# Performance work log

Measured on AMD Instinct MI355X. Metric: run time of the kernel, lower is better.

The kernel has to match this reference:

```python
import jax, jax.numpy as jnp
import numpy as np

N_NODES = 50000
N_EDGES = 400000
LATENT = 128
HIDDEN = 512
N_HEADS = 2          # latent // 64, NodeAttn default num_heads
HEAD_DIM = LATENT // N_HEADS
N_GRAPHS = 500
LN_EPS = 1e-5


def setup_inputs() -> dict:
    key = jax.random.key(0)
    ks = jax.random.split(key, 24)
    s = 0.02
    inp = {
        "edges": jax.random.randint(ks[0], (2, N_EDGES), 0, N_NODES, dtype=jnp.int32),
        "node_feat": jax.random.normal(ks[1], (N_NODES, LATENT), jnp.float32),
        "edge_attr": jax.random.normal(ks[2], (N_EDGES, LATENT), jnp.float32),
        "u": jax.random.normal(ks[3], (N_GRAPHS, LATENT), jnp.float32),
        "num_nodes": jnp.full((N_GRAPHS,), N_NODES // N_GRAPHS, jnp.int32),
        # NodeAttn params (shared for sent/received calls, as in the module)
        "w1": jax.random.normal(ks[4], (3 * LATENT, LATENT), jnp.float32) * s,
        "b1": jnp.zeros((LATENT,), jnp.float32),
        "w2": jax.random.normal(ks[5], (N_HEADS, HEAD_DIM), jnp.float32) * s,
        "w3": jax.random.normal(ks[6], (2 * LATENT, LATENT), jnp.float32) * s,
        "b3": jnp.zeros((LATENT,), jnp.float32),
        # Encoder MLP: 4*latent -> hidden -> hidden -> latent, LN before ReLU
        "mw0": jax.random.normal(ks[7], (4 * LATENT, HIDDEN), jnp.float32) * s,
        "mb0": jnp.zeros((HIDDEN,), jnp.float32),
        "ls0": jnp.ones((HIDDEN,), jnp.float32),
        "lb0": jnp.zeros((HIDDEN,), jnp.float32),
        "mw1": jax.random.normal(ks[8], (HIDDEN, HIDDEN), jnp.float32) * s,
        "mb1": jnp.zeros((HIDDEN,), jnp.float32),
        "ls1": jnp.ones((HIDDEN,), jnp.float32),
        "lb1": jnp.zeros((HIDDEN,), jnp.float32),
        "mw2": jax.random.normal(ks[9], (HIDDEN, LATENT), jnp.float32) * s,
        "mb2": jnp.zeros((LATENT,), jnp.float32),
    }
    return inp


def _layer_norm(x, scale, bias):
    mu = jnp.mean(x, axis=-1, keepdims=True)
    var = jnp.mean(jnp.square(x - mu), axis=-1, keepdims=True)
    return (x - mu) * jax.lax.rsqrt(var + LN_EPS) * scale + bias


def _node_attn(q, k, ea, index, n_nodes, w1, b1, w2, w3, b3):
    # per-edge multi-head scores -> segment softmax over destination index -> scatter-add
    h = jax.nn.leaky_relu(jnp.concatenate([q, k, ea], axis=-1) @ w1 + b1, 0.2)
    h = h.reshape(-1, N_HEADS, HEAD_DIM)                    # [E, H, D]
    logits = jnp.einsum("ehd,hd->eh", h, w2)                 # [E, H]
    m = jax.ops.segment_max(logits, index, num_segments=n_nodes)
    m = jnp.where(jnp.isfinite(m), m, 0.0)                   # empty segments
    e = jnp.exp(logits - m[index])
    z = jax.ops.segment_sum(e, index, num_segments=n_nodes)
    alpha = e / (z[index] + 1e-16)                           # [E, H]
    v = (jnp.concatenate([k, ea], axis=-1) @ w3 + b3).reshape(-1, N_HEADS, HEAD_DIM)
    out = jax.ops.segment_sum(alpha[..., None] * v, index, num_segments=n_nodes)
    return out.reshape(n_nodes, LATENT)


def reference(edges, node_feat, edge_attr, u, num_nodes, w1, b1, w2, w3, b3,
              mw0, mb0, ls0, lb0, mw1, mb1, ls1, lb1, mw2, mb2):
    n = node_feat.shape[0]
    row, col = edges[0], edges[1]
    sent = _node_attn(node_feat[row], node_feat[col], edge_attr, row, n, w1, b1, w2, w3, b3)
    recv = _node_attn(node_feat[col], node_feat[row], edge_attr, col, n, w1, b1, w2, w3, b3)
    glob = jnp.repeat(u, num_nodes, axis=0, total_repeat_length=n)
    x = jnp.concatenate([node_feat, sent, recv, glob], axis=1)   # [N, 4*latent]
    h = jax.nn.relu(_layer_norm(x @ mw0 + mb0, ls0, lb0))
    h = jax.nn.relu(_layer_norm(h @ mw1 + mb1, ls1, lb1))
    return h @ mw2 + mb2
```

## Files before the change

### kernel.cpp

```cpp
#include <hip/hip_runtime.h>
#include <math.h>

#define LATENT 128

typedef __attribute__((ext_vector_type(8))) short bf16x8;
typedef __attribute__((ext_vector_type(4))) float f32x4;
typedef __attribute__((ext_vector_type(2))) float f32x2;
typedef __attribute__((ext_vector_type(2))) int i32x2;
typedef __attribute__((ext_vector_type(2))) unsigned u32x2;

union U4B { uint4 u; bf16x8 v; };

template <typename T>
__device__ __forceinline__ T ntl(const T* p) { return __builtin_nontemporal_load(p); }

__device__ __forceinline__ unsigned short f2bf(float f) {
    unsigned int x = __float_as_uint(f);
    unsigned int r = (x + 0x7fffu + ((x >> 16) & 1u)) >> 16;
    return (unsigned short)r;
}
__device__ __forceinline__ float bf2f(unsigned short h) {
    return __uint_as_float(((unsigned int)h) << 16);
}
__device__ __forceinline__ unsigned pk2(float a, float b) {
    return (unsigned)f2bf(a) | ((unsigned)f2bf(b) << 16);
}

__global__ void k_gid(const int* __restrict__ num_nodes, int G, int n, int* __restrict__ gid) {
    __shared__ int goff[1025];
    if (threadIdx.x == 0) {
        int acc = 0;
        for (int g = 0; g < G; ++g) { goff[g] = acc; acc += num_nodes[g]; }
        goff[G] = acc;
    }
    __syncthreads();
    for (int g = 0; g < G; ++g) {
        int s = goff[g];
        int e = goff[g + 1]; if (e > n) e = n;
        for (int i = s + (int)threadIdx.x; i < e; i += blockDim.x) gid[i] = g;
    }
}

#define FN  1152
#define FE3 1248
#define FEV 1280
__global__ __launch_bounds__(256) void k_pack2(const float* __restrict__ mw0,
                                               const float* __restrict__ mw1,
                                               const float* __restrict__ mw2,
                                               const float* __restrict__ w1,
                                               const float* __restrict__ w3,
                                               uint4* __restrict__ pw) {
    int tid = blockIdx.x * 256 + threadIdx.x;
    if (tid >= 1312 * 64) return;
    int fid = tid >> 6, lane = tid & 63;
    const float* src; int kt, nt, N;
    if (fid < 512)       { src = mw0;            kt = fid >> 5;           nt = fid & 31;           N = 512; }
    else if (fid < 1024) { src = mw1;            kt = (fid - 512) >> 5;   nt = (fid - 512) & 31;   N = 512; }
    else if (fid < 1152) { src = mw2;            kt = (fid - 1024) >> 3;  nt = (fid - 1024) & 7;   N = 128; }
    else if (fid < 1184) { src = w1;             kt = (fid - 1152) >> 3;  nt = (fid - 1152) & 7;   N = 128; }
    else if (fid < 1216) { src = w1 + 128 * 128; kt = (fid - 1184) >> 3;  nt = (fid - 1184) & 7;   N = 128; }
    else if (fid < 1248) { src = w3;             kt = (fid - 1216) >> 3;  nt = (fid - 1216) & 7;   N = 128; }
    else if (fid < 1280) { src = w1 + 256 * 128; kt = (fid - 1248) >> 3;  nt = (fid - 1248) & 7;   N = 128; }
    else                 { src = w3 + 128 * 128; kt = (fid - 1280) >> 3;  nt = (fid - 1280) & 7;   N = 128; }
    int col = nt * 16 + (lane & 15);
    int k0 = kt * 32 + (lane >> 4) * 8;
    unsigned int w[4];
#pragma unroll
    for (int p = 0; p < 4; ++p) {
        unsigned int lo = f2bf(src[(size_t)(k0 + 2 * p) * N + col]);
        unsigned int hi = f2bf(src[(size_t)(k0 + 2 * p + 1) * N + col]);
        w[p] = lo | (hi << 16);
    }
    pw[(size_t)fid * 64 + lane] = make_uint4(w[0], w[1], w[2], w[3]);
}

__global__ void k_count(const int* __restrict__ edges, int E,
                        int* __restrict__ deg_s, int* __restrict__ deg_r) {
    int e = blockIdx.x * 256 + threadIdx.x;
    if (e < E) { atomicAdd(&deg_s[edges[e]], 1); atomicAdd(&deg_r[edges[E + e]], 1); }
}

__global__ __launch_bounds__(1024) void k_scan(const int* __restrict__ deg, int n,
                                               int* __restrict__ rowptr, int* __restrict__ cursor) {
    __shared__ int part[1025];
    int t = threadIdx.x;
    int chunk = (n + 1023) / 1024;
    int s = t * chunk, epos = s + chunk; if (epos > n) epos = n; if (s > n) s = n;
    int sum = 0;
    for (int i = s; i < epos; ++i) sum += deg[i];
    part[t] = sum;
    __syncthreads();
    if (t == 0) {
        int run = 0;
        for (int i = 0; i < 1024; ++i) { int v = part[i]; part[i] = run; run += v; }
        part[1024] = run;
    }
    __syncthreads();
    int run = part[t];
    for (int i = s; i < epos; ++i) { rowptr[i] = run; cursor[i] = run; run += deg[i]; }
    if (t == 0) rowptr[n] = part[1024];
}

__global__ void k_fill(const int* __restrict__ edges, int E,
                       int* __restrict__ cur_s, int* __restrict__ cur_r,
                       int2* __restrict__ eo_s, int2* __restrict__ eo_r,
                       int* __restrict__ sm_s, int* __restrict__ sm_r) {
    int e = blockIdx.x * 256 + threadIdx.x;
    if (e < E) {
        int r = edges[e], c = edges[E + e];
        int p = atomicAdd(&cur_s[r], 1); eo_s[p] = make_int2(e, c); sm_s[e] = p;
        int q = atomicAdd(&cur_r[c], 1); eo_r[q] = make_int2(e, r); sm_r[e] = q;
    }
}

__global__ __launch_bounds__(512) void k_nodepre2(const float* __restrict__ nf, int n,
                                                  const uint4* __restrict__ pw,
                                                  unsigned short* __restrict__ PQK,
                                                  unsigned short* __restrict__ PVh) {
    __shared__ uint4 xs[32 * 64];
    int t = threadIdx.x, lane = t & 63, w = t >> 6;
    int wr = w >> 2, wc = w & 3, l15 = lane & 15, lg = lane >> 4;
    int base = blockIdx.x * 128;
#pragma unroll
    for (int it = 0; it < 4; ++it) {
        int chunk = t + it * 512;
        int row = chunk >> 4, k8 = chunk & 15, k = k8 * 8;
        int node = base + row;
        f32x4 v0 = (f32x4)(0.f), v1 = (f32x4)(0.f);
        if (node < n) {
            const f32x4* s4 = (const f32x4*)(nf + (size_t)node * 128 + k);
            v0 = ntl(s4); v1 = ntl(s4 + 1);
        }
        uint4 pkv;
        pkv.x = pk2(v0.x, v0.y); pkv.y = pk2(v0.z, v0.w);
        pkv.z = pk2(v1.x, v1.y); pkv.w = pk2(v1.z, v1.w);
        int kt = k >> 5, g = (k >> 3) & 3;
        xs[(kt * 8 + (row >> 4)) * 64 + g * 16 + (row & 15)] = pkv;
    }
    __syncthreads();
    f32x4 acc[4][6];
#pragma unroll
    for (int rt = 0; rt < 4; ++rt)
#pragma unroll
        for (int ct = 0; ct < 6; ++ct) acc[rt][ct] = (f32x4)(0.f);
    for (int kt = 0; kt < 4; ++kt) {
        U4B a[4];
#pragma unroll
        for (int rt = 0; rt < 4; ++rt) a[rt].u = xs[(kt * 8 + wr * 4 + rt) * 64 + lane];
        U4B b[6];
#pragma unroll
        for (int ct = 0; ct < 6; ++ct) {
            int nt = wc * 6 + ct;
            int mat = nt >> 3, ntm = nt & 7;
            b[ct].u = pw[(size_t)(FN + mat * 32 + kt * 8 + ntm) * 64 + lane];
        }
#pragma unroll
        for (int rt = 0; rt < 4; ++rt)
#pragma unroll
            for (int ct = 0; ct < 6; ++ct)
                acc[rt][ct] = __builtin_amdgcn_mfma_f32_16x16x32_bf16(a[rt].v, b[ct].v, acc[rt][ct], 0, 0, 0);
    }
#pragma unroll
    for (int rt = 0; rt < 4; ++rt)
#pragma unroll
        for (int ct = 0; ct < 6; ++ct) {
            int nt = wc * 6 + ct;
#pragma unroll
            for (int reg = 0; reg < 4; ++reg) {
                int node = base + (wr * 4 + rt) * 16 + lg * 4 + reg;
                if (node < n) {
                    unsigned short hv = f2bf(acc[rt][ct][reg]);
                    if (nt < 16) PQK[(size_t)node * 256 + nt * 16 + l15] = hv;
                    else         PVh[(size_t)node * 128 + (nt - 16) * 16 + l15] = hv;
                }
            }
        }
}

__global__ __launch_bounds__(256) void k_eproj1(const int* __restrict__ edges,
                                                const float* __restrict__ ea, int E,
                                                const uint4* __restrict__ pw,
                                                const unsigned short* __restrict__ PQK,
                                                const float* __restrict__ b1,
                                                const float* __restrict__ w2,
                                                const int* __restrict__ sm_s,
                                                const int* __restrict__ sm_r,
                                                unsigned short* __restrict__ EVg,
                                                float* __restrict__ ess2, float* __restrict__ ers2) {
    __shared__ uint4 xs[16 * 64];
    __shared__ unsigned short edata[64 * 128];
    int t = threadIdx.x, lane = t & 63, w = t >> 6;
    int wc = w, l15 = lane & 15, lg = lane >> 4;
    int base = blockIdx.x * 64;
#pragma unroll
    for (int it = 0; it < 4; ++it) {
        int chunk = t + it * 256;
        int row = chunk >> 4, k8 = chunk & 15, k = k8 * 8;
        int e = base + row;
        f32x4 v0 = (f32x4)(0.f), v1 = (f32x4)(0.f);
        if (e < E) {
            const f32x4* s4 = (const f32x4*)(ea + (size_t)e * 128 + k);
            v0 = ntl(s4); v1 = ntl(s4 + 1);
        }
        uint4 pkv;
        pkv.x = pk2(v0.x, v0.y); pkv.y = pk2(v0.z, v0.w);
        pkv.z = pk2(v1.x, v1.y); pkv.w = pk2(v1.z, v1.w);
        int kt = k >> 5, g = (k >> 3) & 3;
        xs[(kt * 4 + (row >> 4)) * 64 + g * 16 + (row & 15)] = pkv;
    }
    __syncthreads();
    f32x4 acc[4][4];
#pragma unroll
    for (int rt = 0; rt < 4; ++rt)
#pragma unroll
        for (int ct = 0; ct < 4; ++ct) acc[rt][ct] = (f32x4)(0.f);
    for (int kt = 0; kt < 4; ++kt) {
        U4B a[4];
#pragma unroll
        for (int rt = 0; rt < 4; ++rt) a[rt].u = xs[(kt * 4 + rt) * 64 + lane];
        U4B b[4];
        b[0].u = pw[(size_t)(FE3 + kt * 8 + wc * 2 + 0) * 64 + lane];
        b[1].u = pw[(size_t)(FE3 + kt * 8 + wc * 2 + 1) * 64 + lane];
        b[2].u = pw[(size_t)(FEV + kt * 8 + wc * 2 + 0) * 64 + lane];
        b[3].u = pw[(size_t)(FEV + kt * 8 + wc * 2 + 1) * 64 + lane];
#pragma unroll
        for (int rt = 0; rt < 4; ++rt)
#pragma unroll
            for (int ct = 0; ct < 4; ++ct)
                acc[rt][ct] = __builtin_amdgcn_mfma_f32_16x16x32_bf16(a[rt].v, b[ct].v, acc[rt][ct], 0, 0, 0);
    }
#pragma unroll
    for (int rt = 0; rt < 4; ++rt)
#pragma unroll
        for (int cc = 0; cc < 2; ++cc) {
            int col = (wc * 2 + cc) * 16 + l15;
#pragma unroll
            for (int reg = 0; reg < 4; ++reg) {
                int e_loc = rt * 16 + lg * 4 + reg;
                int e = base + e_loc;
                if (e < E) __builtin_nontemporal_store(f2bf(acc[rt][2 + cc][reg]),
                                                       &EVg[(size_t)e * 128 + col]);
                edata[e_loc * 128 + col] = f2bf(acc[rt][cc][reg]);
            }
        }
    __syncthreads();
    int esub = lane >> 3, dg = lane & 7;
    float b1r[16], w2r[16];
    {
        const float4* b4 = (const float4*)(b1 + dg * 16);
        const float4* w4 = (const float4*)(w2 + (dg >> 2) * 64 + (dg & 3) * 16);
#pragma unroll
        for (int q = 0; q < 4; ++q) {
            float4 bv = b4[q], wv = w4[q];
            b1r[q * 4 + 0] = bv.x; b1r[q * 4 + 1] = bv.y; b1r[q * 4 + 2] = bv.z; b1r[q * 4 + 3] = bv.w;
            w2r[q * 4 + 0] = wv.x; w2r[q * 4 + 1] = wv.y; w2r[q * 4 + 2] = wv.z; w2r[q * 4 + 3] = wv.w;
        }
    }
#pragma unroll
    for (int it = 0; it < 2; ++it) {
        int e_loc = w * 16 + it * 8 + esub;
        int e = base + e_loc;
        if (e >= E) break;
        int r = edges[e], c = edges[E + e];
        const uint4* Aqr = (const uint4*)(PQK + ((size_t)r << 8) + dg * 16);
        const uint4* Akc = (const uint4*)(PQK + ((size_t)c << 8) + 128 + dg * 16);
        const uint4* Aqc = (const uint4*)(PQK + ((size_t)c << 8) + dg * 16);
        const uint4* Akr = (const uint4*)(PQK + ((size_t)r << 8) + 128 + dg * 16);
        const uint4* Ae3 = (const uint4*)(&edata[e_loc * 128 + dg * 16]);
        float ps = 0.f, pr = 0.f;
#pragma unroll
        for (int half = 0; half < 2; ++half) {
            uint4 uqr = Aqr[half], ukc = Akc[half], uqc = Aqc[half], ukr = Akr[half], ue3 = Ae3[half];
            unsigned wqr[4] = {uqr.x, uqr.y, uqr.z, uqr.w};
            unsigned wkc[4] = {ukc.x, ukc.y, ukc.z, ukc.w};
            unsigned wqc[4] = {uqc.x, uqc.y, uqc.z, uqc.w};
            unsigned wkr[4] = {ukr.x, ukr.y, ukr.z, ukr.w};
            unsigned we3[4] = {ue3.x, ue3.y, ue3.z, ue3.w};
#pragma unroll
            for (int q = 0; q < 4; ++q) {
#pragma unroll
                for (int hl = 0; hl < 2; ++hl) {
                    int i = half * 8 + q * 2 + hl;
                    float fqr = hl ? __uint_as_float(wqr[q] & 0xffff0000u) : __uint_as_float(wqr[q] << 16);
                    float fkc = hl ? __uint_as_float(wkc[q] & 0xffff0000u) : __uint_as_float(wkc[q] << 16);
                    float fqc = hl ? __uint_as_float(wqc[q] & 0xffff0000u) : __uint_as_float(wqc[q] << 16);
                    float fkr = hl ? __uint_as_float(wkr[q] & 0xffff0000u) : __uint_as_float(wkr[q] << 16);
                    float fe3 = hl ? __uint_as_float(we3[q] & 0xffff0000u) : __uint_as_float(we3[q] << 16);
                    float com = fe3 + b1r[i];
                    float hs = fqr + fkc + com; hs = hs > 0.f ? hs : 0.2f * hs;
                    float hr = fqc + fkr + com; hr = hr > 0.f ? hr : 0.2f * hr;
                    ps += hs * w2r[i]; pr += hr * w2r[i];
                }
            }
        }
        ps += __shfl_xor(ps, 1); ps += __shfl_xor(ps, 2);
        pr += __shfl_xor(pr, 1); pr += __shfl_xor(pr, 2);
        float Es = expf(ps), Er = expf(pr);
        if (dg == 0) {
            __builtin_nontemporal_store(Es, &ess2[(size_t)sm_s[e] * 2]);
            __builtin_nontemporal_store(Er, &ers2[(size_t)sm_r[e] * 2]);
        } else if (dg == 4) {
            __builtin_nontemporal_store(Es, &ess2[(size_t)sm_s[e] * 2 + 1]);
            __builtin_nontemporal_store(Er, &ers2[(size_t)sm_r[e] * 2 + 1]);
        }
    }
}

__global__ __launch_bounds__(256) void k_aggr(int E, int n,
                                              const int* __restrict__ rps, const int2* __restrict__ eo_s,
                                              const int* __restrict__ rpr, const int2* __restrict__ eo_r,
                                              const float* __restrict__ ess2, const float* __restrict__ ers2,
                                              const unsigned short* __restrict__ PVh,
                                              const unsigned short* __restrict__ EVg,
                                              const float* __restrict__ b3,
                                              unsigned short* __restrict__ out_sh,
                                              unsigned short* __restrict__ out_rh) {
    int w = threadIdx.x >> 6, lane = threadIdx.x & 63;
    int unit = blockIdx.x * 4 + w;
    if (unit >= 2 * n) return;
    bool sent = unit < n;
    int node = sent ? unit : unit - n;
    const int*   rp = sent ? rps : rpr;
    const i32x2* eo = (const i32x2*)(sent ? eo_s : eo_r);
    const float* ex = sent ? ess2 : ers2;
    int s0 = rp[node], s1 = rp[node + 1];
    float b3a = b3[2 * lane], b3b = b3[2 * lane + 1];
    const unsigned* EV32 = (const unsigned*)EVg;
    const unsigned* PV32 = (const unsigned*)PVh;
    float z0 = 0.f, z1 = 0.f, acca = 0.f, accb = 0.f;
    int j = s0;
    for (; j + 4 <= s1; j += 4) {
        i32x2 p[4]; f32x2 ez[4]; unsigned ev[4], pv[4];
#pragma unroll
        for (int q = 0; q < 4; ++q) p[q] = ntl(eo + j + q);
#pragma unroll
        for (int q = 0; q < 4; ++q) ez[q] = ntl((const f32x2*)(ex + 2 * (j + q)));
#pragma unroll
        for (int q = 0; q < 4; ++q) ev[q] = ntl(EV32 + (size_t)p[q].x * 64 + lane);
#pragma unroll
        for (int q = 0; q < 4; ++q) pv[q] = PV32[(size_t)p[q].y * 64 + lane];
#pragma unroll
        for (int q = 0; q < 4; ++q) {
            float va = __uint_as_float(ev[q] << 16) + __uint_as_float(pv[q] << 16) + b3a;
            float vb = __uint_as_float(ev[q] & 0xffff0000u) + __uint_as_float(pv[q] & 0xffff0000u) + b3b;
            z0 += ez[q].x; z1 += ez[q].y;
            float aw = (lane < 32) ? ez[q].x : ez[q].y;
            acca += aw * va; accb += aw * vb;
        }
    }
    for (; j < s1; ++j) {
        i32x2 p = ntl(eo + j);
        f32x2 ez = ntl((const f32x2*)(ex + 2 * j));
        unsigned ev = ntl(EV32 + (size_t)p.x * 64 + lane);
        unsigned pv = PV32[(size_t)p.y * 64 + lane];
        float va = __uint_as_float(ev << 16) + __uint_as_float(pv << 16) + b3a;
        float vb = __uint_as_float(ev & 0xffff0000u) + __uint_as_float(pv & 0xffff0000u) + b3b;
        z0 += ez.x; z1 += ez.y;
        float aw = (lane < 32) ? ez.x : ez.y;
        acca += aw * va; accb += aw * vb;
    }
    float zz = (lane < 32) ? z0 : z1;
    float rz = 1.f / (zz + 1e-16f);
    unsigned o = pk2(acca * rz, accb * rz);
    unsigned* outp = (unsigned*)(sent ? out_sh : out_rh);
    outp[(size_t)node * 64 + lane] = o;
}

__global__ __launch_bounds__(512, 4) void k_mlp3(
    const float* __restrict__ nf, const unsigned short* __restrict__ out_sh,
    const unsigned short* __restrict__ out_rh,
    const float* __restrict__ u, const int* __restrict__ gid, int n,
    const uint4* __restrict__ pw,
    const float* __restrict__ mb0, const float* __restrict__ ls0, const float* __restrict__ lb0,
    const float* __restrict__ mb1, const float* __restrict__ ls1, const float* __restrict__ lb1,
    const float* __restrict__ mb2, float* __restrict__ out) {
    extern __shared__ char smem[];
    char* hx = smem;
    float2* red = (float2*)(smem + 65536);

    int t = threadIdx.x, lane = t & 63, w = t >> 6;
    int wr = w >> 2, wc = w & 3, l15 = lane & 15, lg = lane >> 4;
    int base = blockIdx.x * 64;

#pragma unroll
    for (int it = 0; it < 16; ++it) {
        int chunk = t + it * 512;
        int row = chunk >> 7, kq = chunk & 127;
        int k = kq * 4;
        int node = base + row;
        u32x2 p = (u32x2)(0u);
        if (node < n) {
            int kk = k & 127;
            if (k < 128) {
                f32x4 v = ntl((const f32x4*)(nf + (size_t)node * 128 + kk));
                p.x = pk2(v.x, v.y); p.y = pk2(v.z, v.w);
            } else if (k < 384) {
                const unsigned short* s = (k < 256 ? out_sh : out_rh) + (size_t)node * 128 + kk;
                p = ntl((const u32x2*)s);
            } else {
                f32x4 v = *(const f32x4*)(u + (size_t)gid[node] * 128 + kk);
                p.x = pk2(v.x, v.y); p.y = pk2(v.z, v.w);
            }
        }
        int addr = (row * 1024 + k * 2) ^ ((row & 7) << 4);
        *(u32x2*)(hx + addr) = p;
    }
    __syncthreads();

    f32x4 acc[2][8];
#pragma unroll
    for (int layer = 0; layer < 2; ++layer) {
        const float* MB = layer ? mb1 : mb0;
        const float* LS = layer ? ls1 : ls0;
        const float* LB = layer ? lb1 : lb0;
        const int fbase = layer ? 512 : 0;
#pragma unroll
        for (int rt = 0; rt < 2; ++rt)
#pragma unroll
            for (int ct = 0; ct < 8; ++ct) acc[rt][ct] = (f32x4)(0.f);

        for (int kt = 0; kt < 16; ++kt) {
            U4B b[8];
#pragma unroll
            for (int ct = 0; ct < 8; ++ct)
                b[ct].u = pw[(size_t)(fbase + kt * 32 + wc * 8 + ct) * 64 + lane];
            U4B a[2];
#pragma unroll
            for (int rt = 0; rt < 2; ++rt) {
                int row = wr * 32 + rt * 16 + l15;
                int addr = (row * 1024 + kt * 64 + lg * 16) ^ ((row & 7) << 4);
                a[rt].u = *(const uint4*)(hx + addr);
            }
#pragma unroll
            for (int rt = 0; rt < 2; ++rt)
#pragma unroll
                for (int ct = 0; ct < 8; ++ct)
                    acc[rt][ct] = __builtin_amdgcn_mfma_f32_16x16x32_bf16(a[rt].v, b[ct].v, acc[rt][ct], 0, 0, 0);
        }

        float mbv[8], lsv[8], lbv[8];
#pragma unroll
        for (int ct = 0; ct < 8; ++ct) {
            int col = wc * 128 + ct * 16 + l15;
            mbv[ct] = MB[col]; lsv[ct] = LS[col]; lbv[ct] = LB[col];
        }
#pragma unroll
        for (int rt = 0; rt < 2; ++rt)
#pragma unroll
            for (int reg = 0; reg < 4; ++reg) {
                float p = 0.f, q = 0.f;
#pragma unroll
                for (int ct = 0; ct < 8; ++ct) {
                    float y = acc[rt][ct][reg] + mbv[ct];
                    acc[rt][ct][reg] = y;
                    p += y; q += y * y;
                }
#pragma unroll
                for (int d = 1; d < 16; d <<= 1) { p += __shfl_xor(p, d); q += __shfl_xor(q, d); }
                if (l15 == 0) {
                    int row = wr * 32 + rt * 16 + lg * 4 + reg;
                    red[row * 4 + wc] = make_float2(p, q);
                }
            }
        __syncthreads();
#pragma unroll
        for (int rt = 0; rt < 2; ++rt)
#pragma unroll
            for (int reg = 0; reg < 4; ++reg) {
                int row = wr * 32 + rt * 16 + lg * 4 + reg;
                float2 r0 = red[row * 4 + 0], r1 = red[row * 4 + 1];
                float2 r2 = red[row * 4 + 2], r3 = red[row * 4 + 3];
                float S = r0.x + r1.x + r2.x + r3.x;
                float S2 = r0.y + r1.y + r2.y + r3.y;
                float mu = S * (1.f / 512.f);
                float var = S2 * (1.f / 512.f) - mu * mu;
                float rs = rsqrtf(var + 1e-5f);
                int rswz = (row & 7) << 4;
#pragma unroll
                for (int ct = 0; ct < 8; ++ct) {
                    float h = (acc[rt][ct][reg] - mu) * rs * lsv[ct] + lbv[ct];
                    h = fmaxf(h, 0.f);
                    int col = wc * 128 + ct * 16 + l15;
                    int addr = (row * 1024 + col * 2) ^ rswz;
                    *(unsigned short*)(hx + addr) = f2bf(h);
                }
            }
        __syncthreads();
    }

    f32x4 a2[2][2];
#pragma unroll
    for (int rt = 0; rt < 2; ++rt)
#pragma unroll
        for (int ct = 0; ct < 2; ++ct) a2[rt][ct] = (f32x4)(0.f);
    for (int kt = 0; kt < 16; ++kt) {
        U4B b[2];
#pragma unroll
        for (int ct = 0; ct < 2; ++ct)
            b[ct].u = pw[(size_t)(1024 + kt * 8 + wc * 2 + ct) * 64 + lane];
        U4B a[2];
#pragma unroll
        for (int rt = 0; rt < 2; ++rt) {
            int row = wr * 32 + rt * 16 + l15;
            int addr = (row * 1024 + kt * 64 + lg * 16) ^ ((row & 7) << 4);
            a[rt].u = *(const uint4*)(hx + addr);
        }
#pragma unroll
        for (int rt = 0; rt < 2; ++rt)
#pragma unroll
            for (int ct = 0; ct < 2; ++ct)
                a2[rt][ct] = __builtin_amdgcn_mfma_f32_16x16x32_bf16(a[rt].v, b[ct].v, a2[rt][ct], 0, 0, 0);
    }
    float mb2v[2];
#pragma unroll
    for (int ct = 0; ct < 2; ++ct) mb2v[ct] = mb2[wc * 32 + ct * 16 + l15];
#pragma unroll
    for (int rt = 0; rt < 2; ++rt)
#pragma unroll
        for (int reg = 0; reg < 4; ++reg) {
            int node = base + wr * 32 + rt * 16 + lg * 4 + reg;
            if (node < n) {
#pragma unroll
                for (int ct = 0; ct < 2; ++ct)
                    __builtin_nontemporal_store(a2[rt][ct][reg] + mb2v[ct],
                        &out[(size_t)node * 128 + wc * 32 + ct * 16 + l15]);
            }
        }
}

extern "C" void kernel_launch(void* const* d_in, const int* in_sizes, int n_in,
                              void* d_out, int out_size, void* d_ws, size_t ws_size,
                              hipStream_t stream) {
    const int*   edges     = (const int*)d_in[0];
    const float* nf        = (const float*)d_in[1];
    const float* ea        = (const float*)d_in[2];
    const float* u         = (const float*)d_in[3];
    const int*   num_nodes = (const int*)d_in[4];
    const float* w1  = (const float*)d_in[5];
    const float* b1  = (const float*)d_in[6];
    const float* w2  = (const float*)d_in[7];
    const float* w3  = (const float*)d_in[8];
    const float* b3  = (const float*)d_in[9];
    const float* mw0 = (const float*)d_in[10];
    const float* mb0 = (const float*)d_in[11];
    const float* ls0 = (const float*)d_in[12];
    const float* lb0 = (const float*)d_in[13];
    const float* mw1 = (const float*)d_in[14];
    const float* mb1 = (const float*)d_in[15];
    const float* ls1 = (const float*)d_in[16];
    const float* lb1 = (const float*)d_in[17];
    const float* mw2 = (const float*)d_in[18];
    const float* mb2 = (const float*)d_in[19];

    int E = in_sizes[0] / 2;
    int n = in_sizes[1] / LATENT;
    int G = in_sizes[4];
    float* out = (float*)d_out;

    char* wsb = (char*)d_ws;
    size_t off = 0;
    auto alloc = [&](size_t bytes) { void* p = (void*)(wsb + off); off += (bytes + 15) & ~(size_t)15; return p; };
    uint4*          pw     = (uint4*)alloc((size_t)1312 * 64 * 16);
    unsigned short* PQK    = (unsigned short*)alloc((size_t)n * 256 * 2);
    unsigned short* PVh    = (unsigned short*)alloc((size_t)n * 128 * 2);
    unsigned short* EVg    = (unsigned short*)alloc((size_t)E * 128 * 2);
    float*          ess2   = (float*)alloc((size_t)E * 2 * 4);
    float*          ers2   = (float*)alloc((size_t)E * 2 * 4);
    unsigned short* out_sh = (unsigned short*)alloc((size_t)n * 128 * 2);
    unsigned short* out_rh = (unsigned short*)alloc((size_t)n * 128 * 2);
    int*            gid    = (int*)alloc((size_t)n * 4);
    int*            deg_s  = (int*)alloc((size_t)n * 4);
    int*            deg_r  = (int*)alloc((size_t)n * 4);
    int*            cur_s  = (int*)alloc((size_t)n * 4);
    int*            cur_r  = (int*)alloc((size_t)n * 4);
    int*            rps    = (int*)alloc((size_t)(n + 1) * 4);
    int*            rpr    = (int*)alloc((size_t)(n + 1) * 4);
    int2*           eo_s   = (int2*)alloc((size_t)E * 8);
    int2*           eo_r   = (int2*)alloc((size_t)E * 8);
    int*            sm_s   = (int*)alloc((size_t)E * 4);
    int*            sm_r   = (int*)alloc((size_t)E * 4);

    hipMemsetAsync(deg_s, 0, (size_t)2 * n * 4 + 16, stream);

    hipFuncSetAttribute((const void*)k_mlp3, hipFuncAttributeMaxDynamicSharedMemorySize, 67584);

    k_gid<<<1, 256, 0, stream>>>(num_nodes, G, n, gid);
    k_pack2<<<(1312 * 64 + 255) / 256, 256, 0, stream>>>(mw0, mw1, mw2, w1, w3, pw);
    k_count<<<(E + 255) / 256, 256, 0, stream>>>(edges, E, deg_s, deg_r);
    k_scan<<<1, 1024, 0, stream>>>(deg_s, n, rps, cur_s);
    k_scan<<<1, 1024, 0, stream>>>(deg_r, n, rpr, cur_r);
    k_fill<<<(E + 255) / 256, 256, 0, stream>>>(edges, E, cur_s, cur_r, eo_s, eo_r, sm_s, sm_r);
    k_nodepre2<<<(n + 127) / 128, 512, 0, stream>>>(nf, n, pw, PQK, PVh);
    k_eproj1<<<(E + 63) / 64, 256, 0, stream>>>(edges, ea, E, pw, PQK, b1, w2, sm_s, sm_r,
                                                EVg, ess2, ers2);
    k_aggr<<<(2 * n + 3) / 4, 256, 0, stream>>>(E, n, rps, eo_s, rpr, eo_r,
                                                ess2, ers2, PVh, EVg, b3, out_sh, out_rh);
    k_mlp3<<<(n + 63) / 64, 512, 67584, stream>>>(nf, out_sh, out_rh, u, gid, n, pw,
                                                  mb0, ls0, lb0, mb1, ls1, lb1, mb2, out);
}
```

Measured before the change: 901.1 us.

## Software-pipeline weight loads in MLP kernel and use shuffle-based scan

```diff
diff --git a/kernel.cpp b/kernel.cpp
--- a/kernel.cpp
+++ b/kernel.cpp
@@ -82,23 +82,30 @@
 
 __global__ __launch_bounds__(1024) void k_scan(const int* __restrict__ deg, int n,
                                                int* __restrict__ rowptr, int* __restrict__ cursor) {
-    __shared__ int part[1025];
+    __shared__ int wsum[16];
     int t = threadIdx.x;
     int chunk = (n + 1023) / 1024;
-    int s = t * chunk, epos = s + chunk; if (epos > n) epos = n; if (s > n) s = n;
+    int s = t * chunk; if (s > n) s = n;
+    int epos = s + chunk; if (epos > n) epos = n;
     int sum = 0;
     for (int i = s; i < epos; ++i) sum += deg[i];
-    part[t] = sum;
+    int lane = t & 63, wid = t >> 6;
+    int v = sum;
+#pragma unroll
+    for (int d = 1; d < 64; d <<= 1) { int o = __shfl_up(v, d); if (lane >= d) v += o; }
+    if (lane == 63) wsum[wid] = v;
     __syncthreads();
-    if (t == 0) {
-        int run = 0;
-        for (int i = 0; i < 1024; ++i) { int v = part[i]; part[i] = run; run += v; }
-        part[1024] = run;
+    if (t < 16) {
+        int wv = wsum[t];
+#pragma unroll
+        for (int d = 1; d < 16; d <<= 1) { int o = __shfl_up(wv, d, 16); if (t >= d) wv += o; }
+        wsum[t] = wv;
     }
     __syncthreads();
-    int run = part[t];
+    int woff = wid ? wsum[wid - 1] : 0;
+    int run = v + woff - sum;
     for (int i = s; i < epos; ++i) { rowptr[i] = run; cursor[i] = run; run += deg[i]; }
-    if (t == 0) rowptr[n] = part[1024];
+    if (t == 1023) rowptr[n] = run;
 }
 
 __global__ void k_fill(const int* __restrict__ edges, int E,
@@ -366,7 +373,7 @@
     outp[(size_t)node * 64 + lane] = o;
 }
 
-__global__ __launch_bounds__(512, 4) void k_mlp3(
+__global__ __launch_bounds__(512, 4) void k_mlp4(
     const float* __restrict__ nf, const unsigned short* __restrict__ out_sh,
     const unsigned short* __restrict__ out_rh,
     const float* __restrict__ u, const int* __restrict__ gid, int n,
@@ -413,17 +420,16 @@
         const float* MB = layer ? mb1 : mb0;
         const float* LS = layer ? ls1 : ls0;
         const float* LB = layer ? lb1 : lb0;
-        const int fbase = layer ? 512 : 0;
+        const uint4* PW = pw + ((size_t)(layer ? 512 : 0) + wc * 8) * 64 + lane;
 #pragma unroll
         for (int rt = 0; rt < 2; ++rt)
 #pragma unroll
             for (int ct = 0; ct < 8; ++ct) acc[rt][ct] = (f32x4)(0.f);
 
+        U4B bn0, bn1;
+        bn0.u = PW[0];
+        bn1.u = PW[64];
         for (int kt = 0; kt < 16; ++kt) {
-            U4B b[8];
-#pragma unroll
-            for (int ct = 0; ct < 8; ++ct)
-                b[ct].u = pw[(size_t)(fbase + kt * 32 + wc * 8 + ct) * 64 + lane];
             U4B a[2];
 #pragma unroll
             for (int rt = 0; rt < 2; ++rt) {
@@ -432,10 +438,19 @@
                 a[rt].u = *(const uint4*)(hx + addr);
             }
 #pragma unroll
-            for (int rt = 0; rt < 2; ++rt)
-#pragma unroll
-                for (int ct = 0; ct < 8; ++ct)
-                    acc[rt][ct] = __builtin_amdgcn_mfma_f32_16x16x32_bf16(a[rt].v, b[ct].v, acc[rt][ct], 0, 0, 0);
+            for (int p = 0; p < 4; ++p) {
+                U4B bc0 = bn0, bc1 = bn1;
+                int nkt = kt, np = p + 1;
+                if (np == 4) { np = 0; ++nkt; }
+                if (nkt < 16) {
+                    size_t fo = (size_t)(nkt * 32 + np * 2) * 64;
+                    bn0.u = PW[fo]; bn1.u = PW[fo + 64];
+                }
+                acc[0][p * 2]     = __builtin_amdgcn_mfma_f32_16x16x32_bf16(a[0].v, bc0.v, acc[0][p * 2], 0, 0, 0);
+                acc[0][p * 2 + 1] = __builtin_amdgcn_mfma_f32_16x16x32_bf16(a[0].v, bc1.v, acc[0][p * 2 + 1], 0, 0, 0);
+                acc[1][p * 2]     = __builtin_amdgcn_mfma_f32_16x16x32_bf16(a[1].v, bc0.v, acc[1][p * 2], 0, 0, 0);
+                acc[1][p * 2 + 1] = __builtin_amdgcn_mfma_f32_16x16x32_bf16(a[1].v, bc1.v, acc[1][p * 2 + 1], 0, 0, 0);
+            }
         }
 
         float mbv[8], lsv[8], lbv[8];
@@ -493,23 +508,28 @@
     for (int rt = 0; rt < 2; ++rt)
 #pragma unroll
         for (int ct = 0; ct < 2; ++ct) a2[rt][ct] = (f32x4)(0.f);
-    for (int kt = 0; kt < 16; ++kt) {
-        U4B b[2];
-#pragma unroll
-        for (int ct = 0; ct < 2; ++ct)
-            b[ct].u = pw[(size_t)(1024 + kt * 8 + wc * 2 + ct) * 64 + lane];
-        U4B a[2];
-#pragma unroll
-        for (int rt = 0; rt < 2; ++rt) {
-            int row = wr * 32 + rt * 16 + l15;
-            int addr = (row * 1024 + kt * 64 + lg * 16) ^ ((row & 7) << 4);
-            a[rt].u = *(const uint4*)(hx + addr);
-        }
-#pragma unroll
-        for (int rt = 0; rt < 2; ++rt)
-#pragma unroll
-            for (int ct = 0; ct < 2; ++ct)
-                a2[rt][ct] = __builtin_amdgcn_mfma_f32_16x16x32_bf16(a[rt].v, b[ct].v, a2[rt][ct], 0, 0, 0);
+    {
+        const uint4* PW2 = pw + ((size_t)1024 + wc * 2) * 64 + lane;
+        U4B bn0, bn1;
+        bn0.u = PW2[0]; bn1.u = PW2[64];
+        for (int kt = 0; kt < 16; ++kt) {
+            U4B a[2];
+#pragma unroll
+            for (int rt = 0; rt < 2; ++rt) {
+                int row = wr * 32 + rt * 16 + l15;
+                int addr = (row * 1024 + kt * 64 + lg * 16) ^ ((row & 7) << 4);
+                a[rt].u = *(const uint4*)(hx + addr);
+            }
+            U4B bc0 = bn0, bc1 = bn1;
+            if (kt < 15) {
+                size_t fo = (size_t)((kt + 1) * 8) * 64;
+                bn0.u = PW2[fo]; bn1.u = PW2[fo + 64];
+            }
+            a2[0][0] = __builtin_amdgcn_mfma_f32_16x16x32_bf16(a[0].v, bc0.v, a2[0][0], 0, 0, 0);
+            a2[0][1] = __builtin_amdgcn_mfma_f32_16x16x32_bf16(a[0].v, bc1.v, a2[0][1], 0, 0, 0);
+            a2[1][0] = __builtin_amdgcn_mfma_f32_16x16x32_bf16(a[1].v, bc0.v, a2[1][0], 0, 0, 0);
+            a2[1][1] = __builtin_amdgcn_mfma_f32_16x16x32_bf16(a[1].v, bc1.v, a2[1][1], 0, 0, 0);
+        }
     }
     float mb2v[2];
 #pragma unroll
@@ -582,7 +602,7 @@
 
     hipMemsetAsync(deg_s, 0, (size_t)2 * n * 4 + 16, stream);
 
-    hipFuncSetAttribute((const void*)k_mlp3, hipFuncAttributeMaxDynamicSharedMemorySize, 67584);
+    hipFuncSetAttribute((const void*)k_mlp4, hipFuncAttributeMaxDynamicSharedMemorySize, 67584);
 
     k_gid<<<1, 256, 0, stream>>>(num_nodes, G, n, gid);
     k_pack2<<<(1312 * 64 + 255) / 256, 256, 0, stream>>>(mw0, mw1, mw2, w1, w3, pw);
@@ -595,6 +615,6 @@
                                                 EVg, ess2, ers2);
     k_aggr<<<(2 * n + 3) / 4, 256, 0, stream>>>(E, n, rps, eo_s, rpr, eo_r,
                                                 ess2, ers2, PVh, EVg, b3, out_sh, out_rh);
-    k_mlp3<<<(n + 63) / 64, 512, 67584, stream>>>(nf, out_sh, out_rh, u, gid, n, pw,
+    k_mlp4<<<(n + 63) / 64, 512, 67584, stream>>>(nf, out_sh, out_rh, u, gid, n, pw,
                                                   mb0, ls0, lb0, mb1, ls1, lb1, mb2, out);
 }
```

Result: slower. 934.9 us (+3.7%).

## Double MLP row tile to 128 nodes and parallelize the CSR scan

Applied to the files above, without the earlier changes.

```diff
diff --git a/kernel.cpp b/kernel.cpp
--- a/kernel.cpp
+++ b/kernel.cpp
@@ -82,23 +82,30 @@
 
 __global__ __launch_bounds__(1024) void k_scan(const int* __restrict__ deg, int n,
                                                int* __restrict__ rowptr, int* __restrict__ cursor) {
-    __shared__ int part[1025];
+    __shared__ int wsum[16];
     int t = threadIdx.x;
     int chunk = (n + 1023) / 1024;
-    int s = t * chunk, epos = s + chunk; if (epos > n) epos = n; if (s > n) s = n;
+    int s = t * chunk; if (s > n) s = n;
+    int epos = s + chunk; if (epos > n) epos = n;
     int sum = 0;
     for (int i = s; i < epos; ++i) sum += deg[i];
-    part[t] = sum;
+    int lane = t & 63, wid = t >> 6;
+    int v = sum;
+#pragma unroll
+    for (int d = 1; d < 64; d <<= 1) { int o = __shfl_up(v, d); if (lane >= d) v += o; }
+    if (lane == 63) wsum[wid] = v;
     __syncthreads();
-    if (t == 0) {
-        int run = 0;
-        for (int i = 0; i < 1024; ++i) { int v = part[i]; part[i] = run; run += v; }
-        part[1024] = run;
+    if (t < 16) {
+        int wv = wsum[t];
+#pragma unroll
+        for (int d = 1; d < 16; d <<= 1) { int o = __shfl_up(wv, d, 16); if (t >= d) wv += o; }
+        wsum[t] = wv;
     }
     __syncthreads();
-    int run = part[t];
+    int woff = wid ? wsum[wid - 1] : 0;
+    int run = v + woff - sum;
     for (int i = s; i < epos; ++i) { rowptr[i] = run; cursor[i] = run; run += deg[i]; }
-    if (t == 0) rowptr[n] = part[1024];
+    if (t == 1023) rowptr[n] = run;
 }
 
 __global__ void k_fill(const int* __restrict__ edges, int E,
@@ -366,7 +373,7 @@
     outp[(size_t)node * 64 + lane] = o;
 }
 
-__global__ __launch_bounds__(512, 4) void k_mlp3(
+__global__ __launch_bounds__(512, 1) void k_mlp5(
     const float* __restrict__ nf, const unsigned short* __restrict__ out_sh,
     const unsigned short* __restrict__ out_rh,
     const float* __restrict__ u, const int* __restrict__ gid, int n,
@@ -376,14 +383,14 @@
     const float* __restrict__ mb2, float* __restrict__ out) {
     extern __shared__ char smem[];
     char* hx = smem;
-    float2* red = (float2*)(smem + 65536);
+    float2* red = (float2*)(smem + 131072);
 
     int t = threadIdx.x, lane = t & 63, w = t >> 6;
     int wr = w >> 2, wc = w & 3, l15 = lane & 15, lg = lane >> 4;
-    int base = blockIdx.x * 64;
-
-#pragma unroll
-    for (int it = 0; it < 16; ++it) {
+    int base = blockIdx.x * 128;
+
+#pragma unroll
+    for (int it = 0; it < 32; ++it) {
         int chunk = t + it * 512;
         int row = chunk >> 7, kq = chunk & 127;
         int k = kq * 4;
@@ -407,7 +414,7 @@
     }
     __syncthreads();
 
-    f32x4 acc[2][8];
+    f32x4 acc[4][8];
 #pragma unroll
     for (int layer = 0; layer < 2; ++layer) {
         const float* MB = layer ? mb1 : mb0;
@@ -415,7 +422,7 @@
         const float* LB = layer ? lb1 : lb0;
         const int fbase = layer ? 512 : 0;
 #pragma unroll
-        for (int rt = 0; rt < 2; ++rt)
+        for (int rt = 0; rt < 4; ++rt)
 #pragma unroll
             for (int ct = 0; ct < 8; ++ct) acc[rt][ct] = (f32x4)(0.f);
 
@@ -424,15 +431,15 @@
 #pragma unroll
             for (int ct = 0; ct < 8; ++ct)
                 b[ct].u = pw[(size_t)(fbase + kt * 32 + wc * 8 + ct) * 64 + lane];
-            U4B a[2];
-#pragma unroll
-            for (int rt = 0; rt < 2; ++rt) {
-                int row = wr * 32 + rt * 16 + l15;
+            U4B a[4];
+#pragma unroll
+            for (int rt = 0; rt < 4; ++rt) {
+                int row = wr * 64 + rt * 16 + l15;
                 int addr = (row * 1024 + kt * 64 + lg * 16) ^ ((row & 7) << 4);
                 a[rt].u = *(const uint4*)(hx + addr);
             }
 #pragma unroll
-            for (int rt = 0; rt < 2; ++rt)
+            for (int rt = 0; rt < 4; ++rt)
 #pragma unroll
                 for (int ct = 0; ct < 8; ++ct)
                     acc[rt][ct] = __builtin_amdgcn_mfma_f32_16x16x32_bf16(a[rt].v, b[ct].v, acc[rt][ct], 0, 0, 0);
@@ -445,7 +452,7 @@
             mbv[ct] = MB[col]; lsv[ct] = LS[col]; lbv[ct] = LB[col];
         }
 #pragma unroll
-        for (int rt = 0; rt < 2; ++rt)
+        for (int rt = 0; rt < 4; ++rt)
 #pragma unroll
             for (int reg = 0; reg < 4; ++reg) {
                 float p = 0.f, q = 0.f;
@@ -458,16 +465,16 @@
 #pragma unroll
                 for (int d = 1; d < 16; d <<= 1) { p += __shfl_xor(p, d); q += __shfl_xor(q, d); }
                 if (l15 == 0) {
-                    int row = wr * 32 + rt * 16 + lg * 4 + reg;
+                    int row = wr * 64 + rt * 16 + lg * 4 + reg;
                     red[row * 4 + wc] = make_float2(p, q);
                 }
             }
         __syncthreads();
 #pragma unroll
-        for (int rt = 0; rt < 2; ++rt)
+        for (int rt = 0; rt < 4; ++rt)
 #pragma unroll
             for (int reg = 0; reg < 4; ++reg) {
-                int row = wr * 32 + rt * 16 + lg * 4 + reg;
+                int row = wr * 64 + rt * 16 + lg * 4 + reg;
                 float2 r0 = red[row * 4 + 0], r1 = red[row * 4 + 1];
                 float2 r2 = red[row * 4 + 2], r3 = red[row * 4 + 3];
                 float S = r0.x + r1.x + r2.x + r3.x;
@@ -488,9 +495,9 @@
         __syncthreads();
     }
 
-    f32x4 a2[2][2];
-#pragma unroll
-    for (int rt = 0; rt < 2; ++rt)
+    f32x4 a2[4][2];
+#pragma unroll
+    for (int rt = 0; rt < 4; ++rt)
 #pragma unroll
         for (int ct = 0; ct < 2; ++ct) a2[rt][ct] = (f32x4)(0.f);
     for (int kt = 0; kt < 16; ++kt) {
@@ -498,15 +505,15 @@
 #pragma unroll
         for (int ct = 0; ct < 2; ++ct)
             b[ct].u = pw[(size_t)(1024 + kt * 8 + wc * 2 + ct) * 64 + lane];
-        U4B a[2];
-#pragma unroll
-        for (int rt = 0; rt < 2; ++rt) {
-            int row = wr * 32 + rt * 16 + l15;
+        U4B a[4];
+#pragma unroll
+        for (int rt = 0; rt < 4; ++rt) {
+            int row = wr * 64 + rt * 16 + l15;
             int addr = (row * 1024 + kt * 64 + lg * 16) ^ ((row & 7) << 4);
             a[rt].u = *(const uint4*)(hx + addr);
         }
 #pragma unroll
-        for (int rt = 0; rt < 2; ++rt)
+        for (int rt = 0; rt < 4; ++rt)
 #pragma unroll
             for (int ct = 0; ct < 2; ++ct)
                 a2[rt][ct] = __builtin_amdgcn_mfma_f32_16x16x32_bf16(a[rt].v, b[ct].v, a2[rt][ct], 0, 0, 0);
@@ -515,15 +522,14 @@
 #pragma unroll
     for (int ct = 0; ct < 2; ++ct) mb2v[ct] = mb2[wc * 32 + ct * 16 + l15];
 #pragma unroll
-    for (int rt = 0; rt < 2; ++rt)
+    for (int rt = 0; rt < 4; ++rt)
 #pragma unroll
         for (int reg = 0; reg < 4; ++reg) {
-            int node = base + wr * 32 + rt * 16 + lg * 4 + reg;
+            int node = base + wr * 64 + rt * 16 + lg * 4 + reg;
             if (node < n) {
 #pragma unroll
                 for (int ct = 0; ct < 2; ++ct)
-                    __builtin_nontemporal_store(a2[rt][ct][reg] + mb2v[ct],
-                        &out[(size_t)node * 128 + wc * 32 + ct * 16 + l15]);
+                    out[(size_t)node * 128 + wc * 32 + ct * 16 + l15] = a2[rt][ct][reg] + mb2v[ct];
             }
         }
 }
@@ -582,7 +588,7 @@
 
     hipMemsetAsync(deg_s, 0, (size_t)2 * n * 4 + 16, stream);
 
-    hipFuncSetAttribute((const void*)k_mlp3, hipFuncAttributeMaxDynamicSharedMemorySize, 67584);
+    hipFuncSetAttribute((const void*)k_mlp5, hipFuncAttributeMaxDynamicSharedMemorySize, 135168);
 
     k_gid<<<1, 256, 0, stream>>>(num_nodes, G, n, gid);
     k_pack2<<<(1312 * 64 + 255) / 256, 256, 0, stream>>>(mw0, mw1, mw2, w1, w3, pw);
@@ -595,6 +601,6 @@
                                                 EVg, ess2, ers2);
     k_aggr<<<(2 * n + 3) / 4, 256, 0, stream>>>(E, n, rps, eo_s, rpr, eo_r,
                                                 ess2, ers2, PVh, EVg, b3, out_sh, out_rh);
-    k_mlp3<<<(n + 63) / 64, 512, 67584, stream>>>(nf, out_sh, out_rh, u, gid, n, pw,
-                                                  mb0, ls0, lb0, mb1, ls1, lb1, mb2, out);
-}
+    k_mlp5<<<(n + 127) / 128, 512, 135168, stream>>>(nf, out_sh, out_rh, u, gid, n, pw,
+                                                     mb0, ls0, lb0, mb1, ls1, lb1, mb2, out);
+}
```

New measurement: 897.1 us. About the same (-0.4%).

## Stage MLP weight tiles through double-buffered LDS and parallelize scan with shuffles

Applied to the files above, without the earlier changes.

```diff
diff --git a/kernel.cpp b/kernel.cpp
--- a/kernel.cpp
+++ b/kernel.cpp
@@ -82,23 +82,30 @@
 
 __global__ __launch_bounds__(1024) void k_scan(const int* __restrict__ deg, int n,
                                                int* __restrict__ rowptr, int* __restrict__ cursor) {
-    __shared__ int part[1025];
+    __shared__ int wsum[16];
     int t = threadIdx.x;
     int chunk = (n + 1023) / 1024;
-    int s = t * chunk, epos = s + chunk; if (epos > n) epos = n; if (s > n) s = n;
+    int s = t * chunk; if (s > n) s = n;
+    int epos = s + chunk; if (epos > n) epos = n;
     int sum = 0;
     for (int i = s; i < epos; ++i) sum += deg[i];
-    part[t] = sum;
+    int lane = t & 63, wid = t >> 6;
+    int v = sum;
+#pragma unroll
+    for (int d = 1; d < 64; d <<= 1) { int o = __shfl_up(v, d); if (lane >= d) v += o; }
+    if (lane == 63) wsum[wid] = v;
     __syncthreads();
-    if (t == 0) {
-        int run = 0;
-        for (int i = 0; i < 1024; ++i) { int v = part[i]; part[i] = run; run += v; }
-        part[1024] = run;
+    if (t < 16) {
+        int wv = wsum[t];
+#pragma unroll
+        for (int d = 1; d < 16; d <<= 1) { int o = __shfl_up(wv, d, 16); if (t >= d) wv += o; }
+        wsum[t] = wv;
     }
     __syncthreads();
-    int run = part[t];
+    int woff = wid ? wsum[wid - 1] : 0;
+    int run = v + woff - sum;
     for (int i = s; i < epos; ++i) { rowptr[i] = run; cursor[i] = run; run += deg[i]; }
-    if (t == 0) rowptr[n] = part[1024];
+    if (t == 1023) rowptr[n] = run;
 }
 
 __global__ void k_fill(const int* __restrict__ edges, int E,
@@ -366,7 +373,7 @@
     outp[(size_t)node * 64 + lane] = o;
 }
 
-__global__ __launch_bounds__(512, 4) void k_mlp3(
+__global__ __launch_bounds__(512) void k_mlp7(
     const float* __restrict__ nf, const unsigned short* __restrict__ out_sh,
     const unsigned short* __restrict__ out_rh,
     const float* __restrict__ u, const int* __restrict__ gid, int n,
@@ -376,7 +383,8 @@
     const float* __restrict__ mb2, float* __restrict__ out) {
     extern __shared__ char smem[];
     char* hx = smem;
-    float2* red = (float2*)(smem + 65536);
+    char* bb = smem + 65536;
+    float2* red = (float2*)(smem + 131072);
 
     int t = threadIdx.x, lane = t & 63, w = t >> 6;
     int wr = w >> 2, wc = w & 3, l15 = lane & 15, lg = lane >> 4;
@@ -405,6 +413,13 @@
         int addr = (row * 1024 + k * 2) ^ ((row & 7) << 4);
         *(u32x2*)(hx + addr) = p;
     }
+    {
+        uint4 bn[4];
+#pragma unroll
+        for (int q = 0; q < 4; ++q) bn[q] = pw[(size_t)q * 512 + t];
+#pragma unroll
+        for (int q = 0; q < 4; ++q) *(uint4*)(bb + ((size_t)q * 512 + t) * 16) = bn[q];
+    }
     __syncthreads();
 
     f32x4 acc[2][8];
@@ -419,11 +434,19 @@
 #pragma unroll
             for (int ct = 0; ct < 8; ++ct) acc[rt][ct] = (f32x4)(0.f);
 
+        int buf = 0;
         for (int kt = 0; kt < 16; ++kt) {
+            uint4 bn[4];
+            bool pre = (kt < 15);
+            if (pre) {
+                size_t sb = ((size_t)fbase + (size_t)(kt + 1) * 32) * 64;
+#pragma unroll
+                for (int q = 0; q < 4; ++q) bn[q] = pw[sb + (size_t)q * 512 + t];
+            }
             U4B b[8];
 #pragma unroll
             for (int ct = 0; ct < 8; ++ct)
-                b[ct].u = pw[(size_t)(fbase + kt * 32 + wc * 8 + ct) * 64 + lane];
+                b[ct].u = *(const uint4*)(bb + (size_t)buf * 32768 + ((wc * 8 + ct) * 64 + lane) * 16);
             U4B a[2];
 #pragma unroll
             for (int rt = 0; rt < 2; ++rt) {
@@ -436,6 +459,22 @@
 #pragma unroll
                 for (int ct = 0; ct < 8; ++ct)
                     acc[rt][ct] = __builtin_amdgcn_mfma_f32_16x16x32_bf16(a[rt].v, b[ct].v, acc[rt][ct], 0, 0, 0);
+            if (pre) {
+                char* dst = bb + (size_t)(buf ^ 1) * 32768;
+#pragma unroll
+                for (int q = 0; q < 4; ++q) *(uint4*)(dst + ((size_t)q * 512 + t) * 16) = bn[q];
+            }
+            __syncthreads();
+            buf ^= 1;
+        }
+
+        uint4 bnp[4];
+        int nfrag = layer == 0 ? 4 : 1;
+        {
+            size_t sb = layer == 0 ? (size_t)512 * 64 : (size_t)1024 * 64;
+#pragma unroll
+            for (int q = 0; q < 4; ++q)
+                if (q < nfrag) bnp[q] = pw[sb + (size_t)q * 512 + t];
         }
 
         float mbv[8], lsv[8], lbv[8];
@@ -485,6 +524,9 @@
                     *(unsigned short*)(hx + addr) = f2bf(h);
                 }
             }
+#pragma unroll
+        for (int q = 0; q < 4; ++q)
+            if (q < nfrag) *(uint4*)(bb + ((size_t)q * 512 + t) * 16) = bnp[q];
         __syncthreads();
     }
 
@@ -493,23 +535,32 @@
     for (int rt = 0; rt < 2; ++rt)
 #pragma unroll
         for (int ct = 0; ct < 2; ++ct) a2[rt][ct] = (f32x4)(0.f);
-    for (int kt = 0; kt < 16; ++kt) {
-        U4B b[2];
-#pragma unroll
-        for (int ct = 0; ct < 2; ++ct)
-            b[ct].u = pw[(size_t)(1024 + kt * 8 + wc * 2 + ct) * 64 + lane];
-        U4B a[2];
-#pragma unroll
-        for (int rt = 0; rt < 2; ++rt) {
-            int row = wr * 32 + rt * 16 + l15;
-            int addr = (row * 1024 + kt * 64 + lg * 16) ^ ((row & 7) << 4);
-            a[rt].u = *(const uint4*)(hx + addr);
-        }
-#pragma unroll
-        for (int rt = 0; rt < 2; ++rt)
+    {
+        int buf = 0;
+        for (int kt = 0; kt < 16; ++kt) {
+            uint4 bn;
+            bool pre = (kt < 15);
+            if (pre) bn = pw[((size_t)1024 + (size_t)(kt + 1) * 8) * 64 + t];
+            U4B b[2];
 #pragma unroll
             for (int ct = 0; ct < 2; ++ct)
-                a2[rt][ct] = __builtin_amdgcn_mfma_f32_16x16x32_bf16(a[rt].v, b[ct].v, a2[rt][ct], 0, 0, 0);
+                b[ct].u = *(const uint4*)(bb + (size_t)buf * 32768 + ((wc * 2 + ct) * 64 + lane) * 16);
+            U4B a[2];
+#pragma unroll
+            for (int rt = 0; rt < 2; ++rt) {
+                int row = wr * 32 + rt * 16 + l15;
+                int addr = (row * 1024 + kt * 64 + lg * 16) ^ ((row & 7) << 4);
+                a[rt].u = *(const uint4*)(hx + addr);
+            }
+#pragma unroll
+            for (int rt = 0; rt < 2; ++rt)
+#pragma unroll
+                for (int ct = 0; ct < 2; ++ct)
+                    a2[rt][ct] = __builtin_amdgcn_mfma_f32_16x16x32_bf16(a[rt].v, b[ct].v, a2[rt][ct], 0, 0, 0);
+            if (pre) *(uint4*)(bb + (size_t)(buf ^ 1) * 32768 + (size_t)t * 16) = bn;
+            __syncthreads();
+            buf ^= 1;
+        }
     }
     float mb2v[2];
 #pragma unroll
@@ -582,7 +633,7 @@
 
     hipMemsetAsync(deg_s, 0, (size_t)2 * n * 4 + 16, stream);
 
-    hipFuncSetAttribute((const void*)k_mlp3, hipFuncAttributeMaxDynamicSharedMemorySize, 67584);
+    hipFuncSetAttribute((const void*)k_mlp7, hipFuncAttributeMaxDynamicSharedMemorySize, 133120);
 
     k_gid<<<1, 256, 0, stream>>>(num_nodes, G, n, gid);
     k_pack2<<<(1312 * 64 + 255) / 256, 256, 0, stream>>>(mw0, mw1, mw2, w1, w3, pw);
@@ -595,6 +646,6 @@
                                                 EVg, ess2, ers2);
     k_aggr<<<(2 * n + 3) / 4, 256, 0, stream>>>(E, n, rps, eo_s, rpr, eo_r,
                                                 ess2, ers2, PVh, EVg, b3, out_sh, out_rh);
-    k_mlp3<<<(n + 63) / 64, 512, 67584, stream>>>(nf, out_sh, out_rh, u, gid, n, pw,
-                                                  mb0, ls0, lb0, mb1, ls1, lb1, mb2, out);
-}
+    k_mlp7<<<(n + 63) / 64, 512, 133120, stream>>>(nf, out_sh, out_rh, u, gid, n, pw,
+                                                   mb0, ls0, lb0, mb1, ls1, lb1, mb2, out);
+}
```

After: 864.7 us. -4.0%, faster.
